# Performance work log

Measured on AMD Instinct MI355X. Metric: run time of the kernel, lower is better.

Reference implementation:

```python
import jax, jax.numpy as jnp
import numpy as np

B, N, D = 64, 8192, 128
IN, OUT, H = 64, 64, 512
NH_R, NH_W = 4, 4
GD_R = D + 6          # k, beta, g, s(3), gamma
GD_W = 3 * D + 6      # + erase, add
LSTM_IN = IN + OUT + NH_R * D
EPS = 1e-10


def setup_inputs() -> dict:
    key = jax.random.key(0)
    ks = jax.random.split(key, 18)
    f32 = jnp.float32

    def nrm(k, shape, scale=1.0):
        return (jax.random.normal(k, shape) * scale).astype(f32)

    mem_dev = 1.0 / float(np.sqrt(N + D))   # matches NTMMemory.initialize_memory scale
    return {
        'x_input': nrm(ks[0], (B, IN)),
        'prev_y': nrm(ks[1], (B, OUT)),
        'prev_read': nrm(ks[2], (B, NH_R * D), 0.1),
        'memory': nrm(ks[3], (B, N, D), mem_dev),
        'prev_w_read': jax.nn.softmax(nrm(ks[4], (B, NH_R, N)), axis=-1),
        'prev_w_write': jax.nn.softmax(nrm(ks[5], (B, NH_W, N)), axis=-1),
        'h0': nrm(ks[6], (B, H), 0.1),
        'c0': nrm(ks[7], (B, H), 0.1),
        'W_ih': nrm(ks[8], (4 * H, LSTM_IN), 1.0 / np.sqrt(LSTM_IN)),
        'W_hh': nrm(ks[9], (4 * H, H), 1.0 / np.sqrt(H)),
        'b_ih': jnp.zeros((4 * H,), f32),
        'b_hh': jnp.zeros((4 * H,), f32),
        'W_rhead': nrm(ks[10], (NH_R * GD_R, H), 1.0 / np.sqrt(H)),
        'b_rhead': jnp.zeros((NH_R * GD_R,), f32),
        'W_whead': nrm(ks[11], (NH_W * GD_W, H), 1.0 / np.sqrt(H)),
        'b_whead': jnp.zeros((NH_W * GD_W,), f32),
        'W_out': nrm(ks[12], (OUT, H + NH_R * D), 1.0 / np.sqrt(H + NH_R * D)),
        'b_out': jnp.zeros((OUT,), f32),
    }


def _address(ctrl, W, b, nh, gd, memory, prev_w):
    """Content + location addressing for nh heads. ctrl:[B,H] -> w:[B,nh,N]."""
    o = (ctrl @ W.T + b).reshape(ctrl.shape[0], nh, gd)
    k = o[..., :D]                                          # [B,nh,D]
    beta = jax.nn.softplus(o[..., D:D + 1])
    g = jax.nn.sigmoid(o[..., D + 1:D + 2])
    s = jax.nn.softmax(jax.nn.softplus(o[..., D + 2:D + 5]), axis=-1)  # 3-way shift
    gamma = 1.0 + jax.nn.softplus(o[..., D + 5:D + 6])
    # batched cosine similarity (replaces triple python loop in source)
    kn = k / (jnp.linalg.norm(k, axis=-1, keepdims=True) + EPS)
    mn = memory / (jnp.linalg.norm(memory, axis=-1, keepdims=True) + EPS)
    sim = jnp.einsum('bhd,bnd->bhn', kn, mn)                # [B,nh,N]
    wc = jax.nn.softmax(beta * sim, axis=-1)
    # interpolation + circular convolution shift (shifts -1,0,+1)
    wg = g * wc + (1.0 - g) * prev_w
    ws = (s[..., 0:1] * jnp.roll(wg, 1, axis=-1)
          + s[..., 1:2] * wg
          + s[..., 2:3] * jnp.roll(wg, -1, axis=-1))
    # sharpening
    wp = ws ** gamma
    w = wp / (jnp.sum(wp, axis=-1, keepdims=True) + EPS)
    return w, o


def reference(x_input, prev_y, prev_read, memory, prev_w_read, prev_w_write,
              h0, c0, W_ih, W_hh, b_ih, b_hh,
              W_rhead, b_rhead, W_whead, b_whead, W_out, b_out):
    # --- controller: one LSTM step (PyTorch gate order i,f,g,o) ---
    ctrl_in = jnp.concatenate([x_input, prev_y, prev_read], axis=-1)   # [B,LSTM_IN]
    gates = ctrl_in @ W_ih.T + b_ih + h0 @ W_hh.T + b_hh               # [B,4H]
    i, f, gg, o = jnp.split(gates, 4, axis=-1)
    c = jax.nn.sigmoid(f) * c0 + jax.nn.sigmoid(i) * jnp.tanh(gg)
    h = jax.nn.sigmoid(o) * jnp.tanh(c)
    # --- write heads: address then erase/add (batched outer products) ---
    w_w, ow = _address(h, W_whead, b_whead, NH_W, GD_W, memory, prev_w_write)
    erase = ow[..., D + 6:2 * D + 6]       # raw slices, as in source _generate_addressing
    add = ow[..., 2 * D + 6:3 * D + 6]
    mem = memory
    for hidx in range(NH_W):               # small fixed head count
        wv = w_w[:, hidx, :, None]         # [B,N,1]
        mem = mem * (1.0 - wv * erase[:, hidx, None, :]) + wv * add[:, hidx, None, :]
    # --- read heads ---
    w_r, _ = _address(h, W_rhead, b_rhead, NH_R, GD_R, mem, prev_w_read)
    r = jnp.einsum('bhn,bnd->bhd', w_r, mem)                # [B,NH_R,D]
    # --- external output fn ---
    ext_in = jnp.concatenate([h, r.reshape(r.shape[0], NH_R * D)], axis=-1)
    y = jnp.tanh(ext_in @ W_out.T + b_out)                  # [B,OUT]
    return (y, mem, h, c, w_r, w_w)
```

## Files before the change

kernel.cpp:

```cpp
#include <hip/hip_runtime.h>
#include <math.h>

#define B 64
#define N 8192
#define D 128
#define H 512
#define NHEAD 4
#define GDW 390
#define GDR 134
#define KL 1152
#define EPSF 1e-10f

typedef float f4 __attribute__((ext_vector_type(4)));

__device__ __forceinline__ float softplusf(float x) {
    return x > 20.f ? x : log1pf(expf(x));
}
__device__ __forceinline__ float sigmoidf(float x) {
    return 1.f / (1.f + expf(-x));
}
__device__ __forceinline__ f4 ntload4(const float* p) {
    return __builtin_nontemporal_load((const f4*)p);
}
__device__ __forceinline__ void ntstore4(float* p, f4 v) {
    __builtin_nontemporal_store(v, (f4*)p);
}

__global__ void prep_xt(const float* __restrict__ x, const float* __restrict__ py,
                        const float* __restrict__ pr, const float* __restrict__ h0,
                        float* __restrict__ XT) {
    int idx = blockIdx.x * 256 + threadIdx.x;
    if (idx >= KL * B) return;
    int k = idx >> 6, b = idx & 63;
    float v;
    if (k < 64)       v = x[b * 64 + k];
    else if (k < 128) v = py[b * 64 + (k - 64)];
    else if (k < 640) v = pr[b * 512 + (k - 128)];
    else              v = h0[b * 512 + (k - 640)];
    XT[idx] = v;
}

__global__ __launch_bounds__(256) void controller(const float* __restrict__ XT,
        const float* __restrict__ W_ih, const float* __restrict__ W_hh,
        const float* __restrict__ b_ih, const float* __restrict__ b_hh,
        float* __restrict__ gatesT) {
    __shared__ float xs[64 * 64];
    int tid = threadIdx.x;
    int lane = tid & 63;
    int wave = tid >> 6;
    int j0 = blockIdx.x * 16 + wave * 4;
    float acc[4] = {0.f, 0.f, 0.f, 0.f};
    for (int k0 = 0; k0 < KL; k0 += 64) {
        __syncthreads();
        #pragma unroll
        for (int i = 0; i < 16; i++) xs[tid + i * 256] = XT[k0 * 64 + tid + i * 256];
        __syncthreads();
        const float* wp[4];
        #pragma unroll
        for (int jj = 0; jj < 4; jj++) {
            int j = j0 + jj;
            wp[jj] = (k0 < 640) ? (W_ih + j * 640 + k0) : (W_hh + j * 512 + (k0 - 640));
        }
        #pragma unroll 4
        for (int k = 0; k < 64; k++) {
            float xv = xs[k * 64 + lane];
            #pragma unroll
            for (int jj = 0; jj < 4; jj++) acc[jj] = fmaf(wp[jj][k], xv, acc[jj]);
        }
    }
    #pragma unroll
    for (int jj = 0; jj < 4; jj++) {
        int j = j0 + jj;
        gatesT[j * 64 + lane] = acc[jj] + b_ih[j] + b_hh[j];
    }
}

__global__ void lstm_cell(const float* __restrict__ gatesT, const float* __restrict__ c0,
                          float* __restrict__ h_out, float* __restrict__ c_out,
                          float* __restrict__ HT) {
    int tid = blockIdx.x * 256 + threadIdx.x;
    int b = tid >> 9, u = tid & 511;
    float gi = gatesT[u * 64 + b];
    float gf = gatesT[(512 + u) * 64 + b];
    float gg = gatesT[(1024 + u) * 64 + b];
    float go = gatesT[(1536 + u) * 64 + b];
    float c = sigmoidf(gf) * c0[b * 512 + u] + sigmoidf(gi) * tanhf(gg);
    float h = sigmoidf(go) * tanhf(c);
    c_out[b * 512 + u] = c;
    h_out[b * 512 + u] = h;
    HT[u * 64 + b] = h;
}

__global__ __launch_bounds__(256) void head_proj(const float* __restrict__ HT,
        const float* __restrict__ W_w, const float* __restrict__ W_r,
        const float* __restrict__ b_w, const float* __restrict__ b_r,
        float* __restrict__ o_w, float* __restrict__ o_r) {
    __shared__ float xs[64 * 64];
    int tid = threadIdx.x;
    int lane = tid & 63;
    int wave = tid >> 6;
    int j0 = blockIdx.x * 16 + wave * 4;
    float acc[4] = {0.f, 0.f, 0.f, 0.f};
    const float* wp[4];
    #pragma unroll
    for (int jj = 0; jj < 4; jj++) {
        int j = j0 + jj;
        wp[jj] = (j < 1560) ? (W_w + j * 512) : (W_r + (j - 1560) * 512);
    }
    for (int k0 = 0; k0 < 512; k0 += 64) {
        __syncthreads();
        #pragma unroll
        for (int i = 0; i < 16; i++) xs[tid + i * 256] = HT[k0 * 64 + tid + i * 256];
        __syncthreads();
        #pragma unroll 4
        for (int k = 0; k < 64; k++) {
            float xv = xs[k * 64 + lane];
            #pragma unroll
            for (int jj = 0; jj < 4; jj++) acc[jj] = fmaf(wp[jj][k0 + k], xv, acc[jj]);
        }
    }
    #pragma unroll
    for (int jj = 0; jj < 4; jj++) {
        int j = j0 + jj;
        if (j < 1560) o_w[lane * 1560 + j] = acc[jj] + b_w[j];
        else          o_r[lane * 536 + (j - 1560)] = acc[jj] + b_r[j - 1560];
    }
}

__global__ __launch_bounds__(128) void head_params(const float* __restrict__ o_w,
        const float* __restrict__ o_r, float* __restrict__ knw, float* __restrict__ knr,
        float* __restrict__ pw, float* __restrict__ prd, float* __restrict__ rzero) {
    __shared__ float red[2];
    int id = blockIdx.x;
    if (id < 256) rzero[id * 128 + threadIdx.x] = 0.f;
    bool isw = id < 256;
    int bh = isw ? id : id - 256;
    const float* o = isw ? (o_w + (bh >> 2) * 1560 + (bh & 3) * GDW)
                         : (o_r + (bh >> 2) * 536 + (bh & 3) * GDR);
    float* kn = (isw ? knw : knr) + bh * 128;
    float* pp = (isw ? pw : prd) + bh * 6;
    int t = threadIdx.x;
    float kv = o[t];
    float ss = kv * kv;
    #pragma unroll
    for (int m = 1; m < 64; m <<= 1) ss += __shfl_xor(ss, m);
    if ((t & 63) == 0) red[t >> 6] = ss;
    __syncthreads();
    float norm = sqrtf(red[0] + red[1]);
    kn[t] = kv / (norm + EPSF);
    if (t == 0) {
        float beta = softplusf(o[128]);
        float g = sigmoidf(o[129]);
        float s0 = softplusf(o[130]), s1 = softplusf(o[131]), s2 = softplusf(o[132]);
        float mx = fmaxf(s0, fmaxf(s1, s2));
        float e0 = expf(s0 - mx), e1 = expf(s1 - mx), e2 = expf(s2 - mx);
        float inv = 1.f / (e0 + e1 + e2);
        float gamma = 1.f + softplusf(o[133]);
        pp[0] = beta; pp[1] = g; pp[2] = e0 * inv; pp[3] = e1 * inv; pp[4] = e2 * inv; pp[5] = gamma;
    }
}

__global__ __launch_bounds__(256) void sim_write(const float* __restrict__ mem,
        const float* __restrict__ knw, float* __restrict__ sim) {
    int t = threadIdx.x;
    int lane = t & 63;
    int wv = t >> 6;
    int j = lane & 15;
    int u = lane >> 4;
    int b = blockIdx.x >> 7;
    int nb = (blockIdx.x & 127) * 64 + wv * 16 + u;
    f4 k[4][2];
    #pragma unroll
    for (int h = 0; h < 4; h++) {
        #pragma unroll
        for (int s = 0; s < 2; s++)
            k[h][s] = *(const f4*)(knw + (b * 4 + h) * 128 + s * 64 + j * 4);
    }
    #pragma unroll
    for (int it = 0; it < 4; it++) {
        int n = nb + it * 4;
        size_t base = ((size_t)b * N + n) * D + j * 4;
        const f4 m0 = ntload4(mem + base);
        const f4 m1 = ntload4(mem + base + 64);
        float s0 = m0.x*k[0][0].x + m0.y*k[0][0].y + m0.z*k[0][0].z + m0.w*k[0][0].w
                 + m1.x*k[0][1].x + m1.y*k[0][1].y + m1.z*k[0][1].z + m1.w*k[0][1].w;
        float s1 = m0.x*k[1][0].x + m0.y*k[1][0].y + m0.z*k[1][0].z + m0.w*k[1][0].w
                 + m1.x*k[1][1].x + m1.y*k[1][1].y + m1.z*k[1][1].z + m1.w*k[1][1].w;
        float s2 = m0.x*k[2][0].x + m0.y*k[2][0].y + m0.z*k[2][0].z + m0.w*k[2][0].w
                 + m1.x*k[2][1].x + m1.y*k[2][1].y + m1.z*k[2][1].z + m1.w*k[2][1].w;
        float s3 = m0.x*k[3][0].x + m0.y*k[3][0].y + m0.z*k[3][0].z + m0.w*k[3][0].w
                 + m1.x*k[3][1].x + m1.y*k[3][1].y + m1.z*k[3][1].z + m1.w*k[3][1].w;
        float nn = m0.x*m0.x + m0.y*m0.y + m0.z*m0.z + m0.w*m0.w
                 + m1.x*m1.x + m1.y*m1.y + m1.z*m1.z + m1.w*m1.w;
        s0 += __shfl_xor(s0, 1); s1 += __shfl_xor(s1, 1);
        s2 += __shfl_xor(s2, 1); s3 += __shfl_xor(s3, 1); nn += __shfl_xor(nn, 1);
        float p01 = (j & 1) ? s1 : s0;
        float p23 = (j & 1) ? s3 : s2;
        p01 += __shfl_xor(p01, 2); p23 += __shfl_xor(p23, 2); nn += __shfl_xor(nn, 2);
        float q = (j & 2) ? p23 : p01;
        q += __shfl_xor(q, 4);  nn += __shfl_xor(nn, 4);
        q += __shfl_xor(q, 8);  nn += __shfl_xor(nn, 8);
        if (j < 4) sim[((size_t)(b * 4 + j)) * N + n] = q / (sqrtf(nn) + EPSF);
    }
}

__global__ __launch_bounds__(512) void addr_finalize(const float* __restrict__ sim,
        const float* __restrict__ prev_w, const float* __restrict__ par,
        float* __restrict__ w_out) {
    __shared__ float buf[N];
    __shared__ float pbuf[N];
    __shared__ float red[24];
    int bh = blockIdx.x;
    int t = threadIdx.x;
    int wv = t >> 6;
    const f4* s4 = (const f4*)(sim + (size_t)bh * N);
    const f4* pw4 = (const f4*)(prev_w + (size_t)bh * N);
    f4* out4 = (f4*)(w_out + (size_t)bh * N);
    float beta = par[bh * 6 + 0], g = par[bh * 6 + 1];
    float s0 = par[bh * 6 + 2], s1 = par[bh * 6 + 3], s2 = par[bh * 6 + 4];
    float gamma = par[bh * 6 + 5];
    float mx = -INFINITY;
    #pragma unroll
    for (int c = t; c < N / 4; c += 512) {
        f4 v = s4[c];
        v.x *= beta; v.y *= beta; v.z *= beta; v.w *= beta;
        *(f4*)(buf + c * 4) = v;
        mx = fmaxf(mx, fmaxf(fmaxf(v.x, v.y), fmaxf(v.z, v.w)));
    }
    #pragma unroll
    for (int m = 1; m < 64; m <<= 1) mx = fmaxf(mx, __shfl_xor(mx, m));
    if ((t & 63) == 0) red[wv] = mx;
    __syncthreads();
    mx = red[0];
    #pragma unroll
    for (int kk = 1; kk < 8; kk++) mx = fmaxf(mx, red[kk]);
    float sum = 0.f;
    for (int i = t; i < N; i += 512) {
        float v = expf(buf[i] - mx);
        buf[i] = v;
        sum += v;
    }
    #pragma unroll
    for (int m = 1; m < 64; m <<= 1) sum += __shfl_xor(sum, m);
    if ((t & 63) == 0) red[8 + wv] = sum;
    __syncthreads();
    sum = red[8] + red[9] + red[10] + red[11] + red[12] + red[13] + red[14] + red[15];
    float inv = 1.f / sum;
    #pragma unroll
    for (int c = t; c < N / 4; c += 512) {
        f4 p = pw4[c];
        f4 w;
        w.x = g * (buf[c * 4 + 0] * inv) + (1.f - g) * p.x;
        w.y = g * (buf[c * 4 + 1] * inv) + (1.f - g) * p.y;
        w.z = g * (buf[c * 4 + 2] * inv) + (1.f - g) * p.z;
        w.w = g * (buf[c * 4 + 3] * inv) + (1.f - g) * p.w;
        *(f4*)(buf + c * 4) = w;
    }
    __syncthreads();
    float psum = 0.f;
    for (int i = t; i < N; i += 512) {
        float wsv = s0 * buf[(i + N - 1) & (N - 1)] + s1 * buf[i] + s2 * buf[(i + 1) & (N - 1)];
        float pv = powf(wsv, gamma);
        pbuf[i] = pv;
        psum += pv;
    }
    #pragma unroll
    for (int m = 1; m < 64; m <<= 1) psum += __shfl_xor(psum, m);
    if ((t & 63) == 0) red[16 + wv] = psum;
    __syncthreads();
    psum = red[16] + red[17] + red[18] + red[19] + red[20] + red[21] + red[22] + red[23];
    float rinv = 1.f / (psum + EPSF);
    #pragma unroll
    for (int c = t; c < N / 4; c += 512) {
        f4 o;
        o.x = pbuf[c * 4 + 0] * rinv;
        o.y = pbuf[c * 4 + 1] * rinv;
        o.z = pbuf[c * 4 + 2] * rinv;
        o.w = pbuf[c * 4 + 3] * rinv;
        out4[c] = o;
    }
}

__global__ __launch_bounds__(256) void mem_update(const float* __restrict__ mem_in,
        const float* __restrict__ o_w, const float* __restrict__ w_w,
        const float* __restrict__ knr, float* __restrict__ mem_out,
        float* __restrict__ simr) {
    __shared__ float wlds[4][64];
    int t = threadIdx.x;
    int l = t & 31;
    int rg = t >> 5;
    int b = blockIdx.x >> 7;
    int n0 = (blockIdx.x & 127) * 64;
    {
        int h = t >> 6, idx = t & 63;
        wlds[h][idx] = w_w[((size_t)(b * 4 + h)) * N + n0 + idx];
    }
    f4 e[4], a[4], kr[4];
    #pragma unroll
    for (int h = 0; h < 4; h++) {
        const float* ob = o_w + b * 1560 + h * GDW;
        e[h].x = ob[134 + l * 4 + 0]; e[h].y = ob[134 + l * 4 + 1];
        e[h].z = ob[134 + l * 4 + 2]; e[h].w = ob[134 + l * 4 + 3];
        a[h].x = ob[262 + l * 4 + 0]; a[h].y = ob[262 + l * 4 + 1];
        a[h].z = ob[262 + l * 4 + 2]; a[h].w = ob[262 + l * 4 + 3];
        kr[h] = *(const f4*)(knr + (b * 4 + h) * 128 + l * 4);
    }
    __syncthreads();
    #pragma unroll
    for (int it = 0; it < 8; it++) {
        int n = n0 + it * 8 + rg;
        size_t base = ((size_t)b * N + n) * D + l * 4;
        f4 m = ntload4(mem_in + base);
        #pragma unroll
        for (int h = 0; h < 4; h++) {
            float wv = wlds[h][it * 8 + rg];
            m.x = m.x * (1.f - wv * e[h].x) + wv * a[h].x;
            m.y = m.y * (1.f - wv * e[h].y) + wv * a[h].y;
            m.z = m.z * (1.f - wv * e[h].z) + wv * a[h].z;
            m.w = m.w * (1.f - wv * e[h].w) + wv * a[h].w;
        }
        ntstore4(mem_out + base, m);
        float s0 = m.x * kr[0].x + m.y * kr[0].y + m.z * kr[0].z + m.w * kr[0].w;
        float s1 = m.x * kr[1].x + m.y * kr[1].y + m.z * kr[1].z + m.w * kr[1].w;
        float s2 = m.x * kr[2].x + m.y * kr[2].y + m.z * kr[2].z + m.w * kr[2].w;
        float s3 = m.x * kr[3].x + m.y * kr[3].y + m.z * kr[3].z + m.w * kr[3].w;
        float nn = m.x * m.x + m.y * m.y + m.z * m.z + m.w * m.w;
        s0 += __shfl_xor(s0, 1); s1 += __shfl_xor(s1, 1);
        s2 += __shfl_xor(s2, 1); s3 += __shfl_xor(s3, 1); nn += __shfl_xor(nn, 1);
        float p01 = (l & 1) ? s1 : s0;
        float p23 = (l & 1) ? s3 : s2;
        p01 += __shfl_xor(p01, 2); p23 += __shfl_xor(p23, 2); nn += __shfl_xor(nn, 2);
        float q = (l & 2) ? p23 : p01;
        q += __shfl_xor(q, 4); nn += __shfl_xor(nn, 4);
        float z = (l & 4) ? nn : q;
        z += __shfl_xor(z, 8);
        z += __shfl_xor(z, 16);
        float nnv = __shfl_xor(z, 4);
        if (l < 4) simr[((size_t)(b * 4 + l)) * N + n] = z / (sqrtf(nnv) + EPSF);
    }
}

__global__ __launch_bounds__(256) void read_vec(const float* __restrict__ mem,
        const float* __restrict__ w_r, float* __restrict__ r) {
    __shared__ float lds[8 * 512];
    __shared__ float wlds[4][512];
    int t = threadIdx.x;
    int l = t & 31;
    int rg = t >> 5;
    int b = blockIdx.x >> 4;
    int n0 = (blockIdx.x & 15) * 512;
    for (int i = t; i < 2048; i += 256) {
        int h = i >> 9, idx = i & 511;
        wlds[h][idx] = w_r[((size_t)(b * 4 + h)) * N + n0 + idx];
    }
    __syncthreads();
    f4 acc[4];
    #pragma unroll
    for (int h = 0; h < 4; h++) acc[h] = (f4){0.f, 0.f, 0.f, 0.f};
    #pragma unroll 4
    for (int it = 0; it < 64; it++) {
        int nl = it * 8 + rg;
        const f4 m = ntload4(mem + ((size_t)b * N + n0 + nl) * D + l * 4);
        #pragma unroll
        for (int h = 0; h < 4; h++) {
            float wv = wlds[h][nl];
            acc[h].x += wv * m.x;
            acc[h].y += wv * m.y;
            acc[h].z += wv * m.z;
            acc[h].w += wv * m.w;
        }
    }
    #pragma unroll
    for (int h = 0; h < 4; h++) *(f4*)(lds + rg * 512 + h * 128 + l * 4) = acc[h];
    __syncthreads();
    for (int o = t; o < 512; o += 256) {
        float sum = 0.f;
        #pragma unroll
        for (int g2 = 0; g2 < 8; g2++) sum += lds[g2 * 512 + o];
        atomicAdd(&r[b * 512 + o], sum);
    }
}

__global__ __launch_bounds__(64) void out_y(const float* __restrict__ h,
        const float* __restrict__ r, const float* __restrict__ W_out,
        const float* __restrict__ b_out, float* __restrict__ y) {
    int b = blockIdx.x >> 6;
    int j = blockIdx.x & 63;
    int l = threadIdx.x;
    float acc = 0.f;
    #pragma unroll
    for (int kk = 0; kk < 16; kk++) {
        int k = l + kk * 64;
        float x = (k < 512) ? h[b * 512 + k] : r[b * 512 + (k - 512)];
        acc = fmaf(W_out[j * 1024 + k], x, acc);
    }
    #pragma unroll
    for (int m = 1; m < 64; m <<= 1) acc += __shfl_xor(acc, m);
    if (l == 0) y[b * 64 + j] = tanhf(acc + b_out[j]);
}

extern "C" void kernel_launch(void* const* d_in, const int* in_sizes, int n_in,
                              void* d_out, int out_size, void* d_ws, size_t ws_size,
                              hipStream_t stream) {
    const float* x_input      = (const float*)d_in[0];
    const float* prev_y       = (const float*)d_in[1];
    const float* prev_read    = (const float*)d_in[2];
    const float* memory       = (const float*)d_in[3];
    const float* prev_w_read  = (const float*)d_in[4];
    const float* prev_w_write = (const float*)d_in[5];
    const float* h0           = (const float*)d_in[6];
    const float* c0           = (const float*)d_in[7];
    const float* W_ih         = (const float*)d_in[8];
    const float* W_hh         = (const float*)d_in[9];
    const float* b_ih         = (const float*)d_in[10];
    const float* b_hh         = (const float*)d_in[11];
    const float* W_rhead      = (const float*)d_in[12];
    const float* b_rhead      = (const float*)d_in[13];
    const float* W_whead      = (const float*)d_in[14];
    const float* b_whead      = (const float*)d_in[15];
    const float* W_out        = (const float*)d_in[16];
    const float* b_out        = (const float*)d_in[17];

    float* out = (float*)d_out;
    float* y_o   = out;
    float* mem_o = out + 4096;
    float* h_o   = out + 4096 + 67108864;
    float* c_o   = h_o + 32768;
    float* wr_o  = c_o + 32768;
    float* ww_o  = wr_o + 2097152;

    float* ws     = (float*)d_ws;
    float* XT     = ws;
    float* HT     = XT + 73728;
    float* gatesT = HT + 32768;
    float* o_w    = gatesT + 131072;
    float* o_r    = o_w + 99840;
    float* knw    = o_r + 34304;
    float* knr    = knw + 32768;
    float* pw     = knr + 32768;
    float* prd    = pw + 1536;
    float* sim_w  = prd + 1536;
    float* sim_r  = sim_w + 2097152;
    float* r_ws   = sim_r + 2097152;

    prep_xt<<<288, 256, 0, stream>>>(x_input, prev_y, prev_read, h0, XT);
    controller<<<128, 256, 0, stream>>>(XT, W_ih, W_hh, b_ih, b_hh, gatesT);
    lstm_cell<<<128, 256, 0, stream>>>(gatesT, c0, h_o, c_o, HT);
    head_proj<<<131, 256, 0, stream>>>(HT, W_whead, W_rhead, b_whead, b_rhead, o_w, o_r);
    head_params<<<512, 128, 0, stream>>>(o_w, o_r, knw, knr, pw, prd, r_ws);
    sim_write<<<8192, 256, 0, stream>>>(memory, knw, sim_w);
    addr_finalize<<<256, 512, 0, stream>>>(sim_w, prev_w_write, pw, ww_o);
    mem_update<<<8192, 256, 0, stream>>>(memory, o_w, ww_o, knr, mem_o, sim_r);
    addr_finalize<<<256, 512, 0, stream>>>(sim_r, prev_w_read, prd, wr_o);
    read_vec<<<1024, 256, 0, stream>>>(mem_o, wr_o, r_ws);
    out_y<<<4096, 64, 0, stream>>>(h_o, r_ws, W_out, b_out, y_o);
}
```

Baseline: 714.0 us.

## Fuse input packing into controller, vectorize weight loads, widen addr_finalize blocks

Folds the prep_xt transpose kernel into the controller's shared-memory staging loop, which removes one launch and one round trip through the workspace. The controller, head_proj and out_y kernels now read weights as float4 vectors instead of scalars. addr_finalize doubles its block size to 1024 threads, so each of its 256 blocks has more waves to hide latency. The gathered staging load in the controller uses scattered, uncoalesced reads, and the dominant memory-bound kernels are left unchanged.

```diff
diff --git a/kernel.cpp b/kernel.cpp
--- a/kernel.cpp
+++ b/kernel.cpp
@@ -26,21 +26,9 @@
     __builtin_nontemporal_store(v, (f4*)p);
 }
 
-__global__ void prep_xt(const float* __restrict__ x, const float* __restrict__ py,
-                        const float* __restrict__ pr, const float* __restrict__ h0,
-                        float* __restrict__ XT) {
-    int idx = blockIdx.x * 256 + threadIdx.x;
-    if (idx >= KL * B) return;
-    int k = idx >> 6, b = idx & 63;
-    float v;
-    if (k < 64)       v = x[b * 64 + k];
-    else if (k < 128) v = py[b * 64 + (k - 64)];
-    else if (k < 640) v = pr[b * 512 + (k - 128)];
-    else              v = h0[b * 512 + (k - 640)];
-    XT[idx] = v;
-}
-
-__global__ __launch_bounds__(256) void controller(const float* __restrict__ XT,
+__global__ __launch_bounds__(256) void controller(const float* __restrict__ x,
+        const float* __restrict__ py, const float* __restrict__ pr,
+        const float* __restrict__ h0,
         const float* __restrict__ W_ih, const float* __restrict__ W_hh,
         const float* __restrict__ b_ih, const float* __restrict__ b_hh,
         float* __restrict__ gatesT) {
@@ -53,7 +41,16 @@
     for (int k0 = 0; k0 < KL; k0 += 64) {
         __syncthreads();
         #pragma unroll
-        for (int i = 0; i < 16; i++) xs[tid + i * 256] = XT[k0 * 64 + tid + i * 256];
+        for (int i = 0; i < 16; i++) {
+            int idx = k0 * 64 + tid + i * 256;
+            int k = idx >> 6, b = idx & 63;
+            float v;
+            if (k < 64)       v = x[b * 64 + k];
+            else if (k < 128) v = py[b * 64 + (k - 64)];
+            else if (k < 640) v = pr[b * 512 + (k - 128)];
+            else              v = h0[b * 512 + (k - 640)];
+            xs[tid + i * 256] = v;
+        }
         __syncthreads();
         const float* wp[4];
         #pragma unroll
@@ -62,10 +59,15 @@
             wp[jj] = (k0 < 640) ? (W_ih + j * 640 + k0) : (W_hh + j * 512 + (k0 - 640));
         }
         #pragma unroll 4
-        for (int k = 0; k < 64; k++) {
-            float xv = xs[k * 64 + lane];
+        for (int k = 0; k < 64; k += 4) {
             #pragma unroll
-            for (int jj = 0; jj < 4; jj++) acc[jj] = fmaf(wp[jj][k], xv, acc[jj]);
+            for (int jj = 0; jj < 4; jj++) {
+                f4 w4 = *(const f4*)(wp[jj] + k);
+                acc[jj] = fmaf(w4.x, xs[(k + 0) * 64 + lane], acc[jj]);
+                acc[jj] = fmaf(w4.y, xs[(k + 1) * 64 + lane], acc[jj]);
+                acc[jj] = fmaf(w4.z, xs[(k + 2) * 64 + lane], acc[jj]);
+                acc[jj] = fmaf(w4.w, xs[(k + 3) * 64 + lane], acc[jj]);
+            }
         }
     }
     #pragma unroll
@@ -113,10 +115,15 @@
         for (int i = 0; i < 16; i++) xs[tid + i * 256] = HT[k0 * 64 + tid + i * 256];
         __syncthreads();
         #pragma unroll 4
-        for (int k = 0; k < 64; k++) {
-            float xv = xs[k * 64 + lane];
+        for (int k = 0; k < 64; k += 4) {
             #pragma unroll
-            for (int jj = 0; jj < 4; jj++) acc[jj] = fmaf(wp[jj][k0 + k], xv, acc[jj]);
+            for (int jj = 0; jj < 4; jj++) {
+                f4 w4 = *(const f4*)(wp[jj] + k0 + k);
+                acc[jj] = fmaf(w4.x, xs[(k + 0) * 64 + lane], acc[jj]);
+                acc[jj] = fmaf(w4.y, xs[(k + 1) * 64 + lane], acc[jj]);
+                acc[jj] = fmaf(w4.z, xs[(k + 2) * 64 + lane], acc[jj]);
+                acc[jj] = fmaf(w4.w, xs[(k + 3) * 64 + lane], acc[jj]);
+            }
         }
     }
     #pragma unroll
@@ -204,12 +211,12 @@
     }
 }
 
-__global__ __launch_bounds__(512) void addr_finalize(const float* __restrict__ sim,
+__global__ __launch_bounds__(1024) void addr_finalize(const float* __restrict__ sim,
         const float* __restrict__ prev_w, const float* __restrict__ par,
         float* __restrict__ w_out) {
     __shared__ float buf[N];
     __shared__ float pbuf[N];
-    __shared__ float red[24];
+    __shared__ float red[48];
     int bh = blockIdx.x;
     int t = threadIdx.x;
     int wv = t >> 6;
@@ -221,7 +228,7 @@
     float gamma = par[bh * 6 + 5];
     float mx = -INFINITY;
     #pragma unroll
-    for (int c = t; c < N / 4; c += 512) {
+    for (int c = t; c < N / 4; c += 1024) {
         f4 v = s4[c];
         v.x *= beta; v.y *= beta; v.z *= beta; v.w *= beta;
         *(f4*)(buf + c * 4) = v;
@@ -233,21 +240,24 @@
     __syncthreads();
     mx = red[0];
     #pragma unroll
-    for (int kk = 1; kk < 8; kk++) mx = fmaxf(mx, red[kk]);
+    for (int kk = 1; kk < 16; kk++) mx = fmaxf(mx, red[kk]);
     float sum = 0.f;
-    for (int i = t; i < N; i += 512) {
+    #pragma unroll
+    for (int i = t; i < N; i += 1024) {
         float v = expf(buf[i] - mx);
         buf[i] = v;
         sum += v;
     }
     #pragma unroll
     for (int m = 1; m < 64; m <<= 1) sum += __shfl_xor(sum, m);
-    if ((t & 63) == 0) red[8 + wv] = sum;
-    __syncthreads();
-    sum = red[8] + red[9] + red[10] + red[11] + red[12] + red[13] + red[14] + red[15];
+    if ((t & 63) == 0) red[16 + wv] = sum;
+    __syncthreads();
+    sum = 0.f;
+    #pragma unroll
+    for (int kk = 0; kk < 16; kk++) sum += red[16 + kk];
     float inv = 1.f / sum;
     #pragma unroll
-    for (int c = t; c < N / 4; c += 512) {
+    for (int c = t; c < N / 4; c += 1024) {
         f4 p = pw4[c];
         f4 w;
         w.x = g * (buf[c * 4 + 0] * inv) + (1.f - g) * p.x;
@@ -258,7 +268,8 @@
     }
     __syncthreads();
     float psum = 0.f;
-    for (int i = t; i < N; i += 512) {
+    #pragma unroll
+    for (int i = t; i < N; i += 1024) {
         float wsv = s0 * buf[(i + N - 1) & (N - 1)] + s1 * buf[i] + s2 * buf[(i + 1) & (N - 1)];
         float pv = powf(wsv, gamma);
         pbuf[i] = pv;
@@ -266,12 +277,14 @@
     }
     #pragma unroll
     for (int m = 1; m < 64; m <<= 1) psum += __shfl_xor(psum, m);
-    if ((t & 63) == 0) red[16 + wv] = psum;
-    __syncthreads();
-    psum = red[16] + red[17] + red[18] + red[19] + red[20] + red[21] + red[22] + red[23];
+    if ((t & 63) == 0) red[32 + wv] = psum;
+    __syncthreads();
+    psum = 0.f;
+    #pragma unroll
+    for (int kk = 0; kk < 16; kk++) psum += red[32 + kk];
     float rinv = 1.f / (psum + EPSF);
     #pragma unroll
-    for (int c = t; c < N / 4; c += 512) {
+    for (int c = t; c < N / 4; c += 1024) {
         f4 o;
         o.x = pbuf[c * 4 + 0] * rinv;
         o.y = pbuf[c * 4 + 1] * rinv;
@@ -389,10 +402,15 @@
     int l = threadIdx.x;
     float acc = 0.f;
     #pragma unroll
-    for (int kk = 0; kk < 16; kk++) {
-        int k = l + kk * 64;
-        float x = (k < 512) ? h[b * 512 + k] : r[b * 512 + (k - 512)];
-        acc = fmaf(W_out[j * 1024 + k], x, acc);
+    for (int kk = 0; kk < 4; kk++) {
+        int k = kk * 256 + l * 4;
+        f4 w4 = *(const f4*)(W_out + j * 1024 + k);
+        f4 x4 = (k < 512) ? *(const f4*)(h + b * 512 + k)
+                          : *(const f4*)(r + b * 512 + (k - 512));
+        acc = fmaf(w4.x, x4.x, acc);
+        acc = fmaf(w4.y, x4.y, acc);
+        acc = fmaf(w4.z, x4.z, acc);
+        acc = fmaf(w4.w, x4.w, acc);
     }
     #pragma unroll
     for (int m = 1; m < 64; m <<= 1) acc += __shfl_xor(acc, m);
@@ -443,15 +461,15 @@
     float* sim_r  = sim_w + 2097152;
     float* r_ws   = sim_r + 2097152;
 
-    prep_xt<<<288, 256, 0, stream>>>(x_input, prev_y, prev_read, h0, XT);
-    controller<<<128, 256, 0, stream>>>(XT, W_ih, W_hh, b_ih, b_hh, gatesT);
+    controller<<<128, 256, 0, stream>>>(x_input, prev_y, prev_read, h0,
+                                        W_ih, W_hh, b_ih, b_hh, gatesT);
     lstm_cell<<<128, 256, 0, stream>>>(gatesT, c0, h_o, c_o, HT);
     head_proj<<<131, 256, 0, stream>>>(HT, W_whead, W_rhead, b_whead, b_rhead, o_w, o_r);
     head_params<<<512, 128, 0, stream>>>(o_w, o_r, knw, knr, pw, prd, r_ws);
     sim_write<<<8192, 256, 0, stream>>>(memory, knw, sim_w);
-    addr_finalize<<<256, 512, 0, stream>>>(sim_w, prev_w_write, pw, ww_o);
+    addr_finalize<<<256, 1024, 0, stream>>>(sim_w, prev_w_write, pw, ww_o);
     mem_update<<<8192, 256, 0, stream>>>(memory, o_w, ww_o, knr, mem_o, sim_r);
-    addr_finalize<<<256, 512, 0, stream>>>(sim_r, prev_w_read, prd, wr_o);
+    addr_finalize<<<256, 1024, 0, stream>>>(sim_r, prev_w_read, prd, wr_o);
     read_vec<<<1024, 256, 0, stream>>>(mem_o, wr_o, r_ws);
     out_y<<<4096, 64, 0, stream>>>(h_o, r_ws, W_out, b_out, y_o);
 }
```

Result: slower. 765.8 us (+7.3%).
